# Kernel tuning notes

Hardware: AMD Instinct MI355X
Metric: run time of the kernel (lower is better)

The kernel has to match this reference:

```python
import jax, jax.numpy as jnp
import numpy as np

# dims
N, M, L, E = 50000, 1024, 3, 200000      # tgt nodes, src nodes, subtokens/node, edges
HID, EMB, VOCAB = 512, 256, 512
N_SLT, N_SRT = 4, 5                       # SLT edge types (messages), SRT edge types (output head)
W_SCALE = 0.02


def setup_inputs() -> dict:
    key = jax.random.key(0)
    ks = jax.random.split(key, 20)
    inp = {
        "tgt_x": jax.random.randint(ks[0], (N, L), 0, VOCAB),
        "x": jax.random.normal(ks[1], (M, HID), jnp.float32),
        "tgt_edge_index": jax.random.randint(ks[2], (2, E), 0, N),
        "tgt_edge_type": jax.random.randint(ks[3], (E,), 0, N_SLT),
        "embed_table": jax.random.normal(ks[4], (VOCAB, EMB), jnp.float32) * W_SCALE,
        # GCN layer 1 (called twice in the original forward) and layer 3 params
        "W_h1": jax.random.normal(ks[5], (EMB, EMB), jnp.float32) * W_SCALE,
        "W_rel1": jax.random.normal(ks[6], (N_SLT, EMB, EMB), jnp.float32) * W_SCALE,
        "W_src1": jax.random.normal(ks[7], (HID, EMB), jnp.float32) * W_SCALE,
        "W_h3": jax.random.normal(ks[8], (EMB, EMB), jnp.float32) * W_SCALE,
        "W_rel3": jax.random.normal(ks[9], (N_SLT, EMB, EMB), jnp.float32) * W_SCALE,
        "W_src3": jax.random.normal(ks[10], (HID, EMB), jnp.float32) * W_SCALE,
        # output heads
        "Wz": jax.random.normal(ks[11], (EMB, VOCAB), jnp.float32) * W_SCALE,
        "bz": jnp.zeros((VOCAB,), jnp.float32),
        "Wg": jax.random.normal(ks[12], (2 * EMB, N_SRT), jnp.float32) * W_SCALE,
        "bg": jnp.zeros((N_SRT,), jnp.float32),
    }
    return inp


def _gcn_layer(x_src, h, edge_index, edge_type, W_h, W_rel, W_src):
    """Relational GCN decoder layer with cross-attention to encoder nodes."""
    k = x_src @ W_src                                   # [M, EMB]
    attn = jax.nn.softmax(h @ k.T / jnp.sqrt(jnp.float32(EMB)), axis=1)  # [N, M]
    ctx = attn @ k                                      # [N, EMB]
    # per-edge-type transform first ([N, T, EMB]), then gather per edge
    h_t = jnp.einsum('nd,tdf->ntf', h, W_rel)           # [N, N_SLT, EMB]
    src, tgt = edge_index[0], edge_index[1]
    msg = h_t[src, edge_type]                           # [E, EMB] gather
    agg = jax.ops.segment_sum(msg, tgt, num_segments=h.shape[0])  # [N, EMB]
    return jax.nn.relu(h @ W_h + agg + ctx)


def reference(tgt_x, x, tgt_edge_index, tgt_edge_type, embed_table,
              W_h1, W_rel1, W_src1, W_h3, W_rel3, W_src3, Wz, bz, Wg, bg):
    # embedding + reduction over subtokens
    h = embed_table[tgt_x].sum(axis=1)                  # [N, EMB]
    # original code calls gcn1 twice, then gcn3 (gcn2 unused in training path)
    h = _gcn_layer(x, h, tgt_edge_index, tgt_edge_type, W_h1, W_rel1, W_src1)
    h = _gcn_layer(x, h, tgt_edge_index, tgt_edge_type, W_h1, W_rel1, W_src1)
    h = _gcn_layer(x, h, tgt_edge_index, tgt_edge_type, W_h3, W_rel3, W_src3)
    # node head
    node_pred = jax.nn.log_softmax(h @ Wz + bz, axis=1)  # [N, VOCAB]
    # edge head: gather [2,E,EMB] -> permute -> [E, 2*EMB]
    ef = h[tgt_edge_index]                               # [2, E, EMB]
    ef = jnp.transpose(ef, (1, 0, 2)).reshape(E, 2 * EMB)
    edge_pred = jax.nn.log_softmax(ef @ Wg + bg, axis=1)  # [E, N_SRT]
    return node_pred, edge_pred
```

## Files before the change

kernel.cpp:

```cpp
#include <hip/hip_runtime.h>
#include <hip/hip_bf16.h>
#include <cstdint>

#define N_NODES 50000
#define M_SRC   1024
#define E_EDGES 200000
#define EMB     256
#define HIDN    512
#define VOCABSZ 512
#define KW      1280

typedef __attribute__((ext_vector_type(8))) short bf16x8;
typedef __attribute__((ext_vector_type(4))) short bf16x4;
typedef __attribute__((ext_vector_type(4))) float f32x4;

__device__ inline short f2b(float f) {
    __hip_bfloat16 b = __float2bfloat16(f);
    return *reinterpret_cast<short*>(&b);
}
__device__ inline float b2f(short s) {
    __hip_bfloat16 b = *reinterpret_cast<__hip_bfloat16*>(&s);
    return __bfloat162float(b);
}

__device__ inline void gload16(const void* g, void* l) {
    __builtin_amdgcn_global_load_lds(
        (const __attribute__((address_space(1))) unsigned int*)g,
        (__attribute__((address_space(3))) unsigned int*)l,
        16, 0, 0);
}

__device__ inline void tr_read2(unsigned addr, bf16x4& lo, bf16x4& hi) {
    asm volatile("ds_read_b64_tr_b16 %0, %2\n\tds_read_b64_tr_b16 %1, %2 offset:512"
                 : "=&v"(lo), "=&v"(hi) : "v"(addr));
}

__global__ void embed_kernel(const int* __restrict__ tgt_x,
                             const float* __restrict__ table,
                             short* __restrict__ h)
{
    int n = blockIdx.x, d = threadIdx.x;
    const int* tx = tgt_x + (size_t)n * 3;
    float s = table[(size_t)tx[0] * EMB + d]
            + table[(size_t)tx[1] * EMB + d]
            + table[(size_t)tx[2] * EMB + d];
    h[(size_t)n * EMB + d] = f2b(s);
}

__global__ void convert_kernel(const float* __restrict__ in, short* __restrict__ out, int n)
{
    int i = blockIdx.x * 256 + threadIdx.x;
    if (i * 4 < n) {
        float4 v = *(const float4*)&in[i * 4];
        short4 o;
        o.x = f2b(v.x); o.y = f2b(v.y); o.z = f2b(v.z); o.w = f2b(v.w);
        *(short4*)&out[i * 4] = o;
    }
}

template<typename TIN>
__global__ void transpose_kernel(const TIN* __restrict__ in, short* __restrict__ out, int R, int C)
{
    __shared__ float t[32][33];
    int tx = threadIdx.x & 31, ty = threadIdx.x >> 5;
    int r0 = blockIdx.y * 32, c0 = blockIdx.x * 32;
#pragma unroll
    for (int i = 0; i < 4; i++) {
        int r = ty + i * 8;
        TIN v = in[(size_t)(r0 + r) * C + c0 + tx];
        if constexpr (sizeof(TIN) == 4) t[r][tx] = v;
        else                            t[r][tx] = b2f(v);
    }
    __syncthreads();
#pragma unroll
    for (int i = 0; i < 4; i++) {
        int r = ty + i * 8;
        out[(size_t)(c0 + r) * R + r0 + tx] = f2b(t[tx][r]);
    }
}

__global__ void transposeW_kernel(const float* __restrict__ Wh1, const float* __restrict__ Wh3,
                                  const float* __restrict__ Wr1, const float* __restrict__ Wr3,
                                  short* __restrict__ Wcat1, short* __restrict__ Wcat3)
{
    __shared__ float t[32][33];
    const int z = blockIdx.z;
    const float* in; short* outp; int coloff;
    if (z == 0)      { in = Wh1;                               outp = Wcat1; coloff = 0; }
    else if (z == 1) { in = Wh3;                               outp = Wcat3; coloff = 0; }
    else if (z < 6)  { in = Wr1 + (size_t)(z - 2) * EMB * EMB; outp = Wcat1; coloff = 256 + (z - 2) * 256; }
    else             { in = Wr3 + (size_t)(z - 6) * EMB * EMB; outp = Wcat3; coloff = 256 + (z - 6) * 256; }
    int tx = threadIdx.x & 31, ty = threadIdx.x >> 5;
    int r0 = blockIdx.y * 32, c0 = blockIdx.x * 32;
#pragma unroll
    for (int i = 0; i < 4; i++) {
        int r = ty + i * 8;
        t[r][tx] = in[(size_t)(r0 + r) * EMB + c0 + tx];
    }
    __syncthreads();
#pragma unroll
    for (int i = 0; i < 4; i++) {
        int r = ty + i * 8;
        outp[(size_t)(c0 + r) * KW + coloff + r0 + tx] = f2b(t[tx][r]);
    }
}

template<int MODE>
__global__ __launch_bounds__(256) void mgemm(
    const short* __restrict__ A, const short* __restrict__ BT,
    void* __restrict__ outp, const float* __restrict__ aux,
    const float* __restrict__ bias, int NR, int K, int J)
{
    __shared__ short As[128 * 40];
    __shared__ short Bs[128 * 40];
    const int tid  = threadIdx.x;
    const int n0   = blockIdx.x * 128;
    const int j0   = blockIdx.y * 128;
    const int lane = tid & 63, wid = tid >> 6;
    const int wr   = wid >> 1, wc = wid & 1;

    f32x4 acc[4][4];
#pragma unroll
    for (int m = 0; m < 4; m++)
#pragma unroll
        for (int n = 0; n < 4; n++) acc[m][n] = (f32x4){0.f, 0.f, 0.f, 0.f};

    for (int kt = 0; kt < K; kt += 32) {
#pragma unroll
        for (int r = 0; r < 2; r++) {
            int idx = tid + r * 256;
            int row = idx >> 2, ko = (idx & 3) * 8;
            int n = n0 + row;
            bf16x8 av = {0, 0, 0, 0, 0, 0, 0, 0};
            if (n < NR) av = *(const bf16x8*)&A[(size_t)n * K + kt + ko];
            *(bf16x8*)&As[row * 40 + ko] = av;
            *(bf16x8*)&Bs[row * 40 + ko] = *(const bf16x8*)&BT[(size_t)(j0 + row) * K + kt + ko];
        }
        __syncthreads();
        bf16x8 af[4], bfr[4];
#pragma unroll
        for (int m = 0; m < 4; m++)
            af[m] = *(const bf16x8*)&As[(wr * 64 + m * 16 + (lane & 15)) * 40 + (lane >> 4) * 8];
#pragma unroll
        for (int n = 0; n < 4; n++)
            bfr[n] = *(const bf16x8*)&Bs[(wc * 64 + n * 16 + (lane & 15)) * 40 + (lane >> 4) * 8];
#pragma unroll
        for (int m = 0; m < 4; m++)
#pragma unroll
            for (int n = 0; n < 4; n++)
                acc[m][n] = __builtin_amdgcn_mfma_f32_16x16x32_bf16(af[m], bfr[n], acc[m][n], 0, 0, 0);
        __syncthreads();
    }

#pragma unroll
    for (int m = 0; m < 4; m++) {
        int rbase = wr * 64 + m * 16 + ((lane >> 4) * 4);
#pragma unroll
        for (int r = 0; r < 4; r++) {
            int n_g = n0 + rbase + r;
            if (n_g >= NR) continue;
#pragma unroll
            for (int nn = 0; nn < 4; nn++) {
                int j_g = j0 + wc * 64 + nn * 16 + (lane & 15);
                ((short*)outp)[(size_t)n_g * J + j_g] = f2b(acc[m][nn][r]);
            }
        }
    }
}

__global__ __launch_bounds__(256) void mgemm_wide(
    const short* __restrict__ A1, const short* __restrict__ A2,
    const short* __restrict__ BT, short* __restrict__ outp,
    const float* __restrict__ aux, int NR)
{
    __shared__ short As[2][4096];
    __shared__ short Bs[2][16384];
    const int tid  = threadIdx.x;
    const int n0   = blockIdx.x * 64;
    const int lane = tid & 63, wid = tid >> 6;
    const int wr   = wid >> 1, wc = wid & 1;
    const int l4 = lane >> 4, l15 = lane & 15;

    auto SOFF = [](int r, int d8) {
        return (d8 & 1) * 8 + (r & 3) * 16 + ((r >> 3) & 3) * 64
             + ((r >> 2) & 1) * 256 + (d8 >> 1) * 512;
    };
    int a_row[2], a_d8[2];
#pragma unroll
    for (int q = 0; q < 2; q++) {
        int cig = tid + q * 256;
        int s = cig >> 8, ci = cig & 255;
        a_d8[q]  = (ci & 1) | (((ci >> 6) & 3) << 1);
        a_row[q] = s * 32 + (((ci >> 1) & 3) | (((ci >> 5) & 1) << 2) | (((ci >> 3) & 3) << 3));
    }
    int b_row[8], b_d8[8];
#pragma unroll
    for (int q = 0; q < 8; q++) {
        int cig = tid + q * 256;
        int s = cig >> 8, ci = cig & 255;
        b_d8[q]  = (ci & 1) | (((ci >> 6) & 3) << 1);
        b_row[q] = s * 32 + (((ci >> 1) & 3) | (((ci >> 5) & 1) << 2) | (((ci >> 3) & 3) << 3));
    }

    f32x4 acc[2][8];
#pragma unroll
    for (int m = 0; m < 2; m++)
#pragma unroll
        for (int n = 0; n < 8; n++) acc[m][n] = (f32x4){0.f, 0.f, 0.f, 0.f};

    auto STAGE = [&](int buf, int kt) {
#pragma unroll
        for (int q = 0; q < 2; q++) {
            int col = kt + a_d8[q] * 8;
            const short* src = (col < 256) ? &A1[(size_t)(n0 + a_row[q]) * 256 + col]
                                           : &A2[(size_t)(n0 + a_row[q]) * 1024 + (col - 256)];
            gload16(src, (char*)&As[buf][0] + q * 4096 + wid * 1024);
        }
#pragma unroll
        for (int q = 0; q < 8; q++) {
            gload16(&BT[(size_t)b_row[q] * KW + kt + b_d8[q] * 8],
                    (char*)&Bs[buf][0] + q * 4096 + wid * 1024);
        }
    };

    STAGE(0, 0);
    __syncthreads();

    for (int t = 0; t < 20; t++) {
        const int cur = t & 1;
        if (t + 1 < 20) STAGE(cur ^ 1, (t + 1) * 64);
#pragma unroll
        for (int kst = 0; kst < 2; kst++) {
            const int d8 = kst * 4 + l4;
            bf16x8 af[2], bfr[8];
#pragma unroll
            for (int m = 0; m < 2; m++)
                af[m] = *(const bf16x8*)&As[cur][wr * 2048 + SOFF(m * 16 + l15, d8)];
#pragma unroll
            for (int n = 0; n < 8; n++) {
                int sb = wc * 4 + (n >> 1);
                int r  = (n & 1) * 16 + l15;
                bfr[n] = *(const bf16x8*)&Bs[cur][sb * 2048 + SOFF(r, d8)];
            }
            __builtin_amdgcn_s_setprio(1);
#pragma unroll
            for (int m = 0; m < 2; m++)
#pragma unroll
                for (int n = 0; n < 8; n++)
                    acc[m][n] = __builtin_amdgcn_mfma_f32_16x16x32_bf16(af[m], bfr[n], acc[m][n], 0, 0, 0);
            __builtin_amdgcn_s_setprio(0);
        }
        __syncthreads();
    }

#pragma unroll
    for (int m = 0; m < 2; m++) {
        int rbase = wr * 32 + m * 16 + l4 * 4;
#pragma unroll
        for (int r = 0; r < 4; r++) {
            int n_g = n0 + rbase + r;
            if (n_g >= NR) continue;
#pragma unroll
            for (int nn = 0; nn < 8; nn++) {
                int j_g = wc * 128 + nn * 16 + l15;
                float v = acc[m][nn][r] + aux[(size_t)n_g * 256 + j_g];
                outp[(size_t)n_g * 256 + j_g] = f2b(fmaxf(v, 0.f));
            }
        }
    }
}

__global__ __launch_bounds__(128, 2) void attn_flash(
    const short* __restrict__ h, const short* __restrict__ kb,
    float* __restrict__ C, int NR)
{
    __shared__ short ks[2][32 * 256];
    __shared__ short Ps[64 * 36];

    const int tid = threadIdx.x;
    const int lane = tid & 63, wv = tid >> 6;
    const int l4 = lane >> 4, l15 = lane & 15;
    const int n0 = blockIdx.x * 64;

    auto LOFF = [](int key, int d8) {
        return (d8 & 1) * 8 + (key & 3) * 16 + ((key >> 3) & 3) * 64
             + ((key >> 2) & 1) * 256 + (d8 >> 1) * 512;
    };
    int keyq[8], d8q[8];
#pragma unroll
    for (int q = 0; q < 8; q++) {
        int ci = wv * 64 + lane + q * 128;
        d8q[q]  = (ci & 1) | ((ci >> 6) << 1);
        keyq[q] = ((ci >> 1) & 3) | (((ci >> 5) & 1) << 2) | (((ci >> 3) & 3) << 3);
    }

    bf16x8 hreg[2][8];
#pragma unroll
    for (int rg = 0; rg < 2; rg++) {
        int n = n0 + wv * 32 + rg * 16 + l15;
        const short* hp = &h[(size_t)(n < NR ? n : 0) * 256 + l4 * 8];
#pragma unroll
        for (int kst = 0; kst < 8; kst++) hreg[rg][kst] = *(const bf16x8*)&hp[kst * 32];
        if (n >= NR) {
#pragma unroll
            for (int kst = 0; kst < 8; kst++) hreg[rg][kst] = (bf16x8){0, 0, 0, 0, 0, 0, 0, 0};
        }
    }

#pragma unroll
    for (int q = 0; q < 8; q++)
        gload16(&kb[(size_t)keyq[q] * 256 + d8q[q] * 8],
                (char*)&ks[0][0] + q * 2048 + wv * 1024);
    __syncthreads();

    const unsigned ksbase = (unsigned)(uintptr_t)&ks[0][0];
    const unsigned trlane = 2u * (unsigned)(l15 + l4 * 64);

    f32x4 oacc[2][16];
#pragma unroll
    for (int rg = 0; rg < 2; rg++)
#pragma unroll
        for (int mm = 0; mm < 16; mm++) oacc[rg][mm] = (f32x4){0.f, 0.f, 0.f, 0.f};
    float lsum[2] = {0.f, 0.f};

    for (int c = 0; c < 32; c++) {
        const int cur = c & 1;
        if (c + 1 < 32) {
            const short* kbn = kb + (size_t)(c + 1) * 32 * 256;
#pragma unroll
            for (int q = 0; q < 8; q++)
                gload16(&kbn[(size_t)keyq[q] * 256 + d8q[q] * 8],
                        (char*)&ks[cur ^ 1][0] + q * 2048 + wv * 1024);
        }

        f32x4 sacc[2][2];
#pragma unroll
        for (int rg = 0; rg < 2; rg++) {
            sacc[rg][0] = (f32x4){0.f, 0.f, 0.f, 0.f};
            sacc[rg][1] = (f32x4){0.f, 0.f, 0.f, 0.f};
        }
        __builtin_amdgcn_s_setprio(1);
#pragma unroll
        for (int kst = 0; kst < 8; kst++) {
#pragma unroll
            for (int m = 0; m < 2; m++) {
                int krow = m * 16 + l15;
                bf16x8 afk = *(const bf16x8*)&ks[cur][LOFF(krow, kst * 4 + l4)];
                sacc[0][m] = __builtin_amdgcn_mfma_f32_16x16x32_bf16(afk, hreg[0][kst], sacc[0][m], 0, 0, 0);
                sacc[1][m] = __builtin_amdgcn_mfma_f32_16x16x32_bf16(afk, hreg[1][kst], sacc[1][m], 0, 0, 0);
            }
        }
        __builtin_amdgcn_s_setprio(0);

#pragma unroll
        for (int rg = 0; rg < 2; rg++) {
            int prow = wv * 32 + rg * 16 + l15;
            float psum = 0.f;
#pragma unroll
            for (int m = 0; m < 2; m++) {
                float p0 = __expf(sacc[rg][m][0] * 0.0625f);
                float p1 = __expf(sacc[rg][m][1] * 0.0625f);
                float p2 = __expf(sacc[rg][m][2] * 0.0625f);
                float p3 = __expf(sacc[rg][m][3] * 0.0625f);
                psum += (p0 + p1) + (p2 + p3);
                short4 pk;
                pk.x = f2b(p0); pk.y = f2b(p1); pk.z = f2b(p2); pk.w = f2b(p3);
                *(short4*)&Ps[prow * 36 + m * 16 + l4 * 4] = pk;
            }
            psum += __shfl_xor(psum, 16);
            psum += __shfl_xor(psum, 32);
            lsum[rg] += psum;
        }

        bf16x8 bf2[2];
#pragma unroll
        for (int rg = 0; rg < 2; rg++)
            bf2[rg] = *(const bf16x8*)&Ps[(wv * 32 + rg * 16 + l15) * 36 + l4 * 8];
        unsigned trb = ksbase + (unsigned)(cur * 16384) + trlane;
#pragma unroll
        for (int g = 0; g < 2; g++) {
            bf16x4 lo[8], hi[8];
#pragma unroll
            for (int q = 0; q < 8; q++)
                tr_read2(trb + (unsigned)((g * 8 + q) * 1024), lo[q], hi[q]);
            asm volatile("s_waitcnt lgkmcnt(0)" ::: "memory");
            __builtin_amdgcn_sched_barrier(0);
            __builtin_amdgcn_s_setprio(1);
#pragma unroll
            for (int q = 0; q < 8; q++) {
                bf16x8 af2;
#pragma unroll
                for (int t2 = 0; t2 < 4; t2++) { af2[t2] = lo[q][t2]; af2[t2 + 4] = hi[q][t2]; }
                oacc[0][g * 8 + q] = __builtin_amdgcn_mfma_f32_16x16x32_bf16(af2, bf2[0], oacc[0][g * 8 + q], 0, 0, 0);
                oacc[1][g * 8 + q] = __builtin_amdgcn_mfma_f32_16x16x32_bf16(af2, bf2[1], oacc[1][g * 8 + q], 0, 0, 0);
            }
            __builtin_amdgcn_s_setprio(0);
        }

        __syncthreads();
    }

#pragma unroll
    for (int rg = 0; rg < 2; rg++) {
        float li = 1.0f / lsum[rg];
        int hr = n0 + wv * 32 + rg * 16 + l15;
        if (hr >= NR) continue;
#pragma unroll
        for (int mm = 0; mm < 16; mm++) {
            float4 v;
            v.x = oacc[rg][mm][0] * li;
            v.y = oacc[rg][mm][1] * li;
            v.z = oacc[rg][mm][2] * li;
            v.w = oacc[rg][mm][3] * li;
            *(float4*)&C[(size_t)hr * 256 + mm * 16 + l4 * 4] = v;
        }
    }
}

__global__ void hist_kernel(const int* __restrict__ ei, int* __restrict__ deg)
{
    int e = blockIdx.x * 256 + threadIdx.x;
    if (e < E_EDGES) atomicAdd(&deg[ei[E_EDGES + e]], 1);
}

__global__ void scan1_kernel(const int* __restrict__ deg, int* __restrict__ incl,
                             int* __restrict__ bsum)
{
    __shared__ int s[256];
    int i = blockIdx.x * 256 + threadIdx.x;
    int v = (i < N_NODES) ? deg[i] : 0;
    s[threadIdx.x] = v;
    __syncthreads();
#pragma unroll
    for (int off = 1; off < 256; off <<= 1) {
        int t = (threadIdx.x >= off) ? s[threadIdx.x - off] : 0;
        __syncthreads();
        s[threadIdx.x] += t;
        __syncthreads();
    }
    if (i < N_NODES) incl[i] = s[threadIdx.x];
    if (threadIdx.x == 255) bsum[blockIdx.x] = s[255];
}

__global__ void scan2_kernel(int* __restrict__ bsum, int nb)
{
    __shared__ int s[256];
    int v = (threadIdx.x < nb) ? bsum[threadIdx.x] : 0;
    s[threadIdx.x] = v;
    __syncthreads();
#pragma unroll
    for (int off = 1; off < 256; off <<= 1) {
        int t = (threadIdx.x >= off) ? s[threadIdx.x - off] : 0;
        __syncthreads();
        s[threadIdx.x] += t;
        __syncthreads();
    }
    if (threadIdx.x < nb) bsum[threadIdx.x] = s[threadIdx.x];
}

__global__ void scan3_kernel(const int* __restrict__ deg, const int* __restrict__ incl,
                             const int* __restrict__ bsum, int* __restrict__ row_ptr,
                             int* __restrict__ cursor)
{
    int i = blockIdx.x * 256 + threadIdx.x;
    if (i >= N_NODES) return;
    int pref = (blockIdx.x > 0) ? bsum[blockIdx.x - 1] : 0;
    int start = pref + incl[i] - deg[i];
    row_ptr[i] = start;
    cursor[i]  = start;
    if (i == N_NODES - 1) row_ptr[N_NODES] = pref + incl[i];
}

__global__ void fill_kernel(const int* __restrict__ ei, const int* __restrict__ et,
                            int* __restrict__ cursor, int* __restrict__ eidx)
{
    int e = blockIdx.x * 256 + threadIdx.x;
    if (e >= E_EDGES) return;
    int tg = ei[E_EDGES + e];
    int slot = atomicAdd(&cursor[tg], 1);
    eidx[slot] = ei[e] | (et[e] << 16);
}

__global__ void agg2_kernel(const int* __restrict__ row_ptr, const int* __restrict__ eidx,
                            const short* __restrict__ h, short* __restrict__ Bagg)
{
    int w = (blockIdx.x * 256 + threadIdx.x) >> 6;
    if (w >= N_NODES) return;
    int lane = threadIdx.x & 63;
    int s0 = row_ptr[w], s1 = row_ptr[w + 1];
    float a0[4] = {0, 0, 0, 0}, a1[4] = {0, 0, 0, 0}, a2[4] = {0, 0, 0, 0}, a3[4] = {0, 0, 0, 0};
    for (int i = s0; i < s1; i++) {
        int p = eidx[i];
        int s = p & 0xFFFF, t = p >> 16;
        short4 g = *(const short4*)&h[(size_t)s * EMB + lane * 4];
        float f0 = b2f(g.x), f1 = b2f(g.y), f2 = b2f(g.z), f3 = b2f(g.w);
        if (t == 0)      { a0[0] += f0; a0[1] += f1; a0[2] += f2; a0[3] += f3; }
        else if (t == 1) { a1[0] += f0; a1[1] += f1; a1[2] += f2; a1[3] += f3; }
        else if (t == 2) { a2[0] += f0; a2[1] += f1; a2[2] += f2; a2[3] += f3; }
        else             { a3[0] += f0; a3[1] += f1; a3[2] += f2; a3[3] += f3; }
    }
    short4 o;
    o.x = f2b(a0[0]); o.y = f2b(a0[1]); o.z = f2b(a0[2]); o.w = f2b(a0[3]);
    *(short4*)&Bagg[(size_t)w * 1024 + 0 * 256 + lane * 4] = o;
    o.x = f2b(a1[0]); o.y = f2b(a1[1]); o.z = f2b(a1[2]); o.w = f2b(a1[3]);
    *(short4*)&Bagg[(size_t)w * 1024 + 1 * 256 + lane * 4] = o;
    o.x = f2b(a2[0]); o.y = f2b(a2[1]); o.z = f2b(a2[2]); o.w = f2b(a2[3]);
    *(short4*)&Bagg[(size_t)w * 1024 + 2 * 256 + lane * 4] = o;
    o.x = f2b(a3[0]); o.y = f2b(a3[1]); o.z = f2b(a3[2]); o.w = f2b(a3[3]);
    *(short4*)&Bagg[(size_t)w * 1024 + 3 * 256 + lane * 4] = o;
}

__global__ __launch_bounds__(512, 2) void head_kernel(
    const short* __restrict__ hmat, const short* __restrict__ WzT,
    const float* __restrict__ bz, float* __restrict__ out, int NR)
{
    __shared__ short hs[64 * 256];
    __shared__ float redm[64 * 8];
    __shared__ float reds[64 * 8];

    const int tid = threadIdx.x;
    const int lane = tid & 63, wv = tid >> 6;
    const int l4 = lane >> 4, l15 = lane & 15;
    const int n0 = blockIdx.x * 64;

#pragma unroll
    for (int i = 0; i < 4; i++) {
        int idx = tid + i * 512;
        int row = idx >> 5, kg = idx & 31;
        bf16x8 v = {0, 0, 0, 0, 0, 0, 0, 0};
        if (n0 + row < NR) v = *(const bf16x8*)&hmat[(size_t)(n0 + row) * 256 + kg * 8];
        *(bf16x8*)&hs[(row * 256 + kg * 8) ^ ((row & 7) << 3)] = v;
    }
    __syncthreads();

    f32x4 acc[4][4];
#pragma unroll
    for (int m = 0; m < 4; m++)
#pragma unroll
        for (int n = 0; n < 4; n++) acc[m][n] = (f32x4){0.f, 0.f, 0.f, 0.f};

#pragma unroll
    for (int kt = 0; kt < 256; kt += 32) {
        bf16x8 af[4], bfr[4];
#pragma unroll
        for (int m = 0; m < 4; m++) {
            int row = m * 16 + l15;
            af[m] = *(const bf16x8*)&hs[(row * 256 + kt + l4 * 8) ^ ((row & 7) << 3)];
        }
#pragma unroll
        for (int n = 0; n < 4; n++) {
            int col = wv * 64 + n * 16 + l15;
            bfr[n] = *(const bf16x8*)&WzT[(size_t)col * 256 + kt + l4 * 8];
        }
#pragma unroll
        for (int m = 0; m < 4; m++)
#pragma unroll
            for (int n = 0; n < 4; n++)
                acc[m][n] = __builtin_amdgcn_mfma_f32_16x16x32_bf16(af[m], bfr[n], acc[m][n], 0, 0, 0);
    }

    float bcol[4];
#pragma unroll
    for (int n = 0; n < 4; n++) bcol[n] = bz[wv * 64 + n * 16 + l15];
#pragma unroll
    for (int m = 0; m < 4; m++)
#pragma unroll
        for (int n = 0; n < 4; n++)
#pragma unroll
            for (int r = 0; r < 4; r++) acc[m][n][r] += bcol[n];

    float lg[4][4];
#pragma unroll
    for (int m = 0; m < 4; m++)
#pragma unroll
        for (int r = 0; r < 4; r++) {
            float v = fmaxf(fmaxf(acc[m][0][r], acc[m][1][r]), fmaxf(acc[m][2][r], acc[m][3][r]));
            v = fmaxf(v, __shfl_xor(v, 1));
            v = fmaxf(v, __shfl_xor(v, 2));
            v = fmaxf(v, __shfl_xor(v, 4));
            v = fmaxf(v, __shfl_xor(v, 8));
            if (l15 == 0) redm[(m * 16 + l4 * 4 + r) * 8 + wv] = v;
        }
    __syncthreads();
#pragma unroll
    for (int m = 0; m < 4; m++)
#pragma unroll
        for (int r = 0; r < 4; r++) {
            int row = m * 16 + l4 * 4 + r;
            float v = redm[row * 8 + 0];
#pragma unroll
            for (int w = 1; w < 8; w++) v = fmaxf(v, redm[row * 8 + w]);
            lg[m][r] = v;
        }
#pragma unroll
    for (int m = 0; m < 4; m++)
#pragma unroll
        for (int r = 0; r < 4; r++) {
            float gm = lg[m][r];
            float s = __expf(acc[m][0][r] - gm) + __expf(acc[m][1][r] - gm)
                    + __expf(acc[m][2][r] - gm) + __expf(acc[m][3][r] - gm);
            s += __shfl_xor(s, 1);
            s += __shfl_xor(s, 2);
            s += __shfl_xor(s, 4);
            s += __shfl_xor(s, 8);
            if (l15 == 0) reds[(m * 16 + l4 * 4 + r) * 8 + wv] = s;
        }
    __syncthreads();
#pragma unroll
    for (int m = 0; m < 4; m++)
#pragma unroll
        for (int r = 0; r < 4; r++) {
            int row = m * 16 + l4 * 4 + r;
            float s = reds[row * 8 + 0];
#pragma unroll
            for (int w = 1; w < 8; w++) s += reds[row * 8 + w];
            lg[m][r] += __logf(s);
        }
#pragma unroll
    for (int m = 0; m < 4; m++)
#pragma unroll
        for (int r = 0; r < 4; r++) {
            int hr = n0 + m * 16 + l4 * 4 + r;
            if (hr >= NR) continue;
#pragma unroll
            for (int n = 0; n < 4; n++)
                out[(size_t)hr * VOCABSZ + wv * 64 + n * 16 + l15] = acc[m][n][r] - lg[m][r];
        }
}

__global__ __launch_bounds__(256) void nodeproj_kernel(
    const short* __restrict__ h, const float* __restrict__ Wg,
    float* __restrict__ eproj)
{
    int lane = threadIdx.x & 63;
    int gw   = (blockIdx.x * 256 + threadIdx.x) >> 6;
    int nw   = (gridDim.x * 256) >> 6;
    float ws[4][5], wt[4][5];
#pragma unroll
    for (int c = 0; c < 4; c++)
#pragma unroll
        for (int j = 0; j < 5; j++) {
            ws[c][j] = Wg[(size_t)(lane * 4 + c) * 5 + j];
            wt[c][j] = Wg[(size_t)(256 + lane * 4 + c) * 5 + j];
        }

    for (int n = gw; n < N_NODES; n += nw) {
        short4 hv = *(const short4*)&h[(size_t)n * EMB + lane * 4];
        float f[4] = { b2f(hv.x), b2f(hv.y), b2f(hv.z), b2f(hv.w) };
        float a[5] = {0, 0, 0, 0, 0}, b[5] = {0, 0, 0, 0, 0};
#pragma unroll
        for (int c = 0; c < 4; c++)
#pragma unroll
            for (int j = 0; j < 5; j++) {
                a[j] += f[c] * ws[c][j];
                b[j] += f[c] * wt[c][j];
            }
#pragma unroll
        for (int j = 0; j < 5; j++)
#pragma unroll
            for (int off = 32; off; off >>= 1) {
                a[j] += __shfl_xor(a[j], off);
                b[j] += __shfl_xor(b[j], off);
            }
        if (lane == 0) {
#pragma unroll
            for (int j = 0; j < 5; j++) {
                eproj[(size_t)n * 10 + j]     = a[j];
                eproj[(size_t)n * 10 + 5 + j] = b[j];
            }
        }
    }
}

__global__ void edge_lsm_kernel(const int* __restrict__ ei,
                                const float* __restrict__ eproj,
                                const float* __restrict__ bg,
                                float* __restrict__ out)
{
    int e = blockIdx.x * 256 + threadIdx.x;
    if (e >= E_EDGES) return;
    int s = ei[e], t = ei[E_EDGES + e];
    const float* ps = &eproj[(size_t)s * 10];
    const float* pt = &eproj[(size_t)t * 10 + 5];
    float z[5];
#pragma unroll
    for (int j = 0; j < 5; j++) z[j] = ps[j] + pt[j] + bg[j];
    float mm = fmaxf(fmaxf(fmaxf(z[0], z[1]), fmaxf(z[2], z[3])), z[4]);
    float ss = __expf(z[0] - mm) + __expf(z[1] - mm) + __expf(z[2] - mm)
             + __expf(z[3] - mm) + __expf(z[4] - mm);
    float lg = mm + __logf(ss);
    float* o = &out[(size_t)e * 5];
#pragma unroll
    for (int j = 0; j < 5; j++) o[j] = z[j] - lg;
}

extern "C" void kernel_launch(void* const* d_in, const int* in_sizes, int n_in,
                              void* d_out, int out_size, void* d_ws, size_t ws_size,
                              hipStream_t stream)
{
    const int*   tgt_x = (const int*)  d_in[0];
    const float* x     = (const float*)d_in[1];
    const int*   ei    = (const int*)  d_in[2];
    const int*   et    = (const int*)  d_in[3];
    const float* table = (const float*)d_in[4];
    const float* Wh1   = (const float*)d_in[5];
    const float* Wrel1 = (const float*)d_in[6];
    const float* Wsrc1 = (const float*)d_in[7];
    const float* Wh3   = (const float*)d_in[8];
    const float* Wrel3 = (const float*)d_in[9];
    const float* Wsrc3 = (const float*)d_in[10];
    const float* Wz    = (const float*)d_in[11];
    const float* bz    = (const float*)d_in[12];
    const float* Wg    = (const float*)d_in[13];
    const float* bg    = (const float*)d_in[14];
    float* out = (float*)d_out;

    short* h_a = (short*)d_ws;
    short* h_b = h_a + (size_t)N_NODES * EMB;
    float* C   = (float*)(h_b + (size_t)N_NODES * EMB);
    short* Bagg = (short*)(C + (size_t)N_NODES * EMB);
    short* k1b = Bagg + (size_t)N_NODES * 1024;
    short* k3b = k1b + M_SRC * EMB;
    short* x_b = k3b + M_SRC * EMB;
    short* WsT1 = x_b + M_SRC * HIDN;
    short* WsT3 = WsT1 + EMB * HIDN;
    short* Wcat1 = WsT3 + EMB * HIDN;
    short* Wcat3 = Wcat1 + EMB * KW;
    short* WzT  = Wcat3 + EMB * KW;
    int* deg     = (int*)(WzT + VOCABSZ * EMB);
    int* incl    = deg + N_NODES;
    int* bsum    = incl + N_NODES;
    int* row_ptr = bsum + 256;
    int* cursor  = row_ptr + N_NODES + 1;
    int* eidx    = cursor + N_NODES;
    float* eproj = (float*)(eidx + E_EDGES);

    const int gN = (N_NODES + 127) / 128;
    const int gN64 = (N_NODES + 63) / 64;
    const int nb1 = (N_NODES + 255) / 256;

    hipMemsetAsync(deg, 0, N_NODES * sizeof(int), stream);
    hist_kernel<<<(E_EDGES + 255) / 256, 256, 0, stream>>>(ei, deg);
    scan1_kernel<<<nb1, 256, 0, stream>>>(deg, incl, bsum);
    scan2_kernel<<<1, 256, 0, stream>>>(bsum, nb1);
    scan3_kernel<<<nb1, 256, 0, stream>>>(deg, incl, bsum, row_ptr, cursor);
    fill_kernel<<<(E_EDGES + 255) / 256, 256, 0, stream>>>(ei, et, cursor, eidx);

    convert_kernel<<<(M_SRC * HIDN / 4 + 255) / 256, 256, 0, stream>>>(x, x_b, M_SRC * HIDN);
    transpose_kernel<float><<<dim3(EMB / 32, HIDN / 32), 256, 0, stream>>>(Wsrc1, WsT1, HIDN, EMB);
    transpose_kernel<float><<<dim3(EMB / 32, HIDN / 32), 256, 0, stream>>>(Wsrc3, WsT3, HIDN, EMB);
    transposeW_kernel<<<dim3(8, 8, 10), 256, 0, stream>>>(Wh1, Wh3, Wrel1, Wrel3, Wcat1, Wcat3);
    transpose_kernel<float><<<dim3(VOCABSZ / 32, EMB / 32), 256, 0, stream>>>(Wz, WzT, EMB, VOCABSZ);

    mgemm<0><<<dim3(M_SRC / 128, EMB / 128), 256, 0, stream>>>(x_b, WsT1, k1b, nullptr, nullptr, M_SRC, HIDN, EMB);
    mgemm<0><<<dim3(M_SRC / 128, EMB / 128), 256, 0, stream>>>(x_b, WsT3, k3b, nullptr, nullptr, M_SRC, HIDN, EMB);

    embed_kernel<<<N_NODES, 256, 0, stream>>>(tgt_x, table, h_a);

    short* h_cur = h_a;
    short* h_nxt = h_b;
    for (int layer = 0; layer < 3; layer++) {
        const short* kb   = (layer < 2) ? k1b   : k3b;
        const short* Wcat = (layer < 2) ? Wcat1 : Wcat3;

        attn_flash<<<gN64, 128, 0, stream>>>(h_cur, kb, C, N_NODES);
        agg2_kernel<<<(N_NODES + 3) / 4, 256, 0, stream>>>(row_ptr, eidx, h_cur, Bagg);
        mgemm_wide<<<dim3(gN64, 1), 256, 0, stream>>>(h_cur, Bagg, Wcat, h_nxt, C, N_NODES);
        short* tmp = h_cur; h_cur = h_nxt; h_nxt = tmp;
    }

    head_kernel<<<gN64, 512, 0, stream>>>(h_cur, WzT, bz, out, N_NODES);

    nodeproj_kernel<<<2048, 256, 0, stream>>>(h_cur, Wg, eproj);
    edge_lsm_kernel<<<(E_EDGES + 255) / 256, 256, 0, stream>>>(ei, eproj, bg,
                                                               out + (size_t)N_NODES * VOCABSZ);
}
```

Before: 769.7 us.

## Fuse edge aggregation into the wide GEMM A-tile staging via per-type CSR

Builds the CSR keyed by (target node, edge type) buckets instead of by target node. The separate aggregation kernel and its large bf16 Bagg intermediate are removed. mgemm_wide now gathers and sums neighbour rows of h directly while staging the aggregated part of the A operand into LDS. This avoids writing and re-reading a 50000x1024 buffer every layer, but it puts dependent, irregular global loads (row_ptr, eidx, h) and synchronous LDS stores into the GEMM's double-buffered pipeline, which may stall the MFMA loop.

```diff
diff --git a/kernel.cpp b/kernel.cpp
--- a/kernel.cpp
+++ b/kernel.cpp
@@ -9,6 +9,7 @@
 #define HIDN    512
 #define VOCABSZ 512
 #define KW      1280
+#define NB2     (N_NODES * 4)
 
 typedef __attribute__((ext_vector_type(8))) short bf16x8;
 typedef __attribute__((ext_vector_type(4))) short bf16x4;
@@ -169,9 +170,9 @@
 }
 
 __global__ __launch_bounds__(256) void mgemm_wide(
-    const short* __restrict__ A1, const short* __restrict__ A2,
-    const short* __restrict__ BT, short* __restrict__ outp,
-    const float* __restrict__ aux, int NR)
+    const short* __restrict__ A1, const short* __restrict__ BT,
+    short* __restrict__ outp, const float* __restrict__ aux,
+    const int* __restrict__ row_ptr2, const int* __restrict__ eidx2, int NR)
 {
     __shared__ short As[2][4096];
     __shared__ short Bs[2][16384];
@@ -209,12 +210,34 @@
         for (int n = 0; n < 8; n++) acc[m][n] = (f32x4){0.f, 0.f, 0.f, 0.f};
 
     auto STAGE = [&](int buf, int kt) {
-#pragma unroll
-        for (int q = 0; q < 2; q++) {
-            int col = kt + a_d8[q] * 8;
-            const short* src = (col < 256) ? &A1[(size_t)(n0 + a_row[q]) * 256 + col]
-                                           : &A2[(size_t)(n0 + a_row[q]) * 1024 + (col - 256)];
-            gload16(src, (char*)&As[buf][0] + q * 4096 + wid * 1024);
+        if (kt < 256) {
+#pragma unroll
+            for (int q = 0; q < 2; q++) {
+                gload16(&A1[(size_t)(n0 + a_row[q]) * 256 + kt + a_d8[q] * 8],
+                        (char*)&As[buf][0] + q * 4096 + wid * 1024);
+            }
+        } else {
+#pragma unroll
+            for (int q = 0; q < 2; q++) {
+                int n = n0 + a_row[q];
+                int col = kt + a_d8[q] * 8 - 256;
+                int ty = col >> 8, d = col & 255;
+                float a8[8] = {0.f, 0.f, 0.f, 0.f, 0.f, 0.f, 0.f, 0.f};
+                if (n < NR) {
+                    int bkt = n * 4 + ty;
+                    int i0 = row_ptr2[bkt], i1 = row_ptr2[bkt + 1];
+                    for (int i = i0; i < i1; i++) {
+                        int src = eidx2[i];
+                        bf16x8 v = *(const bf16x8*)&A1[(size_t)src * 256 + d];
+#pragma unroll
+                        for (int j = 0; j < 8; j++) a8[j] += b2f(v[j]);
+                    }
+                }
+                bf16x8 o;
+#pragma unroll
+                for (int j = 0; j < 8; j++) o[j] = f2b(a8[j]);
+                *(bf16x8*)((char*)&As[buf][0] + q * 4096 + wid * 1024 + lane * 16) = o;
+            }
         }
 #pragma unroll
         for (int q = 0; q < 8; q++) {
@@ -417,97 +440,69 @@
     }
 }
 
-__global__ void hist_kernel(const int* __restrict__ ei, int* __restrict__ deg)
+__global__ void hist2_kernel(const int* __restrict__ ei, const int* __restrict__ et,
+                             int* __restrict__ deg2)
 {
     int e = blockIdx.x * 256 + threadIdx.x;
-    if (e < E_EDGES) atomicAdd(&deg[ei[E_EDGES + e]], 1);
-}
-
-__global__ void scan1_kernel(const int* __restrict__ deg, int* __restrict__ incl,
-                             int* __restrict__ bsum)
-{
-    __shared__ int s[256];
-    int i = blockIdx.x * 256 + threadIdx.x;
-    int v = (i < N_NODES) ? deg[i] : 0;
+    if (e < E_EDGES) atomicAdd(&deg2[ei[E_EDGES + e] * 4 + et[e]], 1);
+}
+
+__global__ void scan1x_kernel(const int* __restrict__ deg2, int* __restrict__ incl2,
+                              int* __restrict__ bsum)
+{
+    __shared__ int s[1024];
+    int i = blockIdx.x * 1024 + threadIdx.x;
+    int v = (i < NB2) ? deg2[i] : 0;
     s[threadIdx.x] = v;
     __syncthreads();
 #pragma unroll
-    for (int off = 1; off < 256; off <<= 1) {
-        int t = (threadIdx.x >= off) ? s[threadIdx.x - off] : 0;
+    for (int off = 1; off < 1024; off <<= 1) {
+        int t = (threadIdx.x >= (unsigned)off) ? s[threadIdx.x - off] : 0;
         __syncthreads();
         s[threadIdx.x] += t;
         __syncthreads();
     }
-    if (i < N_NODES) incl[i] = s[threadIdx.x];
-    if (threadIdx.x == 255) bsum[blockIdx.x] = s[255];
+    if (i < NB2) incl2[i] = s[threadIdx.x];
+    if (threadIdx.x == 1023) bsum[blockIdx.x] = s[1023];
 }
 
 __global__ void scan2_kernel(int* __restrict__ bsum, int nb)
 {
     __shared__ int s[256];
-    int v = (threadIdx.x < nb) ? bsum[threadIdx.x] : 0;
+    int v = (threadIdx.x < (unsigned)nb) ? bsum[threadIdx.x] : 0;
     s[threadIdx.x] = v;
     __syncthreads();
 #pragma unroll
     for (int off = 1; off < 256; off <<= 1) {
-        int t = (threadIdx.x >= off) ? s[threadIdx.x - off] : 0;
+        int t = (threadIdx.x >= (unsigned)off) ? s[threadIdx.x - off] : 0;
         __syncthreads();
         s[threadIdx.x] += t;
         __syncthreads();
     }
-    if (threadIdx.x < nb) bsum[threadIdx.x] = s[threadIdx.x];
-}
-
-__global__ void scan3_kernel(const int* __restrict__ deg, const int* __restrict__ incl,
-                             const int* __restrict__ bsum, int* __restrict__ row_ptr,
-                             int* __restrict__ cursor)
-{
-    int i = blockIdx.x * 256 + threadIdx.x;
-    if (i >= N_NODES) return;
+    if (threadIdx.x < (unsigned)nb) bsum[threadIdx.x] = s[threadIdx.x];
+}
+
+__global__ void scan3x_kernel(const int* __restrict__ deg2, const int* __restrict__ incl2,
+                              const int* __restrict__ bsum, int* __restrict__ row_ptr2,
+                              int* __restrict__ cursor2)
+{
+    int i = blockIdx.x * 1024 + threadIdx.x;
+    if (i >= NB2) return;
     int pref = (blockIdx.x > 0) ? bsum[blockIdx.x - 1] : 0;
-    int start = pref + incl[i] - deg[i];
-    row_ptr[i] = start;
-    cursor[i]  = start;
-    if (i == N_NODES - 1) row_ptr[N_NODES] = pref + incl[i];
-}
-
-__global__ void fill_kernel(const int* __restrict__ ei, const int* __restrict__ et,
-                            int* __restrict__ cursor, int* __restrict__ eidx)
+    int start = pref + incl2[i] - deg2[i];
+    row_ptr2[i] = start;
+    cursor2[i]  = start;
+    if (i == NB2 - 1) row_ptr2[NB2] = pref + incl2[i];
+}
+
+__global__ void fill2_kernel(const int* __restrict__ ei, const int* __restrict__ et,
+                             int* __restrict__ cursor2, int* __restrict__ eidx2)
 {
     int e = blockIdx.x * 256 + threadIdx.x;
     if (e >= E_EDGES) return;
-    int tg = ei[E_EDGES + e];
-    int slot = atomicAdd(&cursor[tg], 1);
-    eidx[slot] = ei[e] | (et[e] << 16);
-}
-
-__global__ void agg2_kernel(const int* __restrict__ row_ptr, const int* __restrict__ eidx,
-                            const short* __restrict__ h, short* __restrict__ Bagg)
-{
-    int w = (blockIdx.x * 256 + threadIdx.x) >> 6;
-    if (w >= N_NODES) return;
-    int lane = threadIdx.x & 63;
-    int s0 = row_ptr[w], s1 = row_ptr[w + 1];
-    float a0[4] = {0, 0, 0, 0}, a1[4] = {0, 0, 0, 0}, a2[4] = {0, 0, 0, 0}, a3[4] = {0, 0, 0, 0};
-    for (int i = s0; i < s1; i++) {
-        int p = eidx[i];
-        int s = p & 0xFFFF, t = p >> 16;
-        short4 g = *(const short4*)&h[(size_t)s * EMB + lane * 4];
-        float f0 = b2f(g.x), f1 = b2f(g.y), f2 = b2f(g.z), f3 = b2f(g.w);
-        if (t == 0)      { a0[0] += f0; a0[1] += f1; a0[2] += f2; a0[3] += f3; }
-        else if (t == 1) { a1[0] += f0; a1[1] += f1; a1[2] += f2; a1[3] += f3; }
-        else if (t == 2) { a2[0] += f0; a2[1] += f1; a2[2] += f2; a2[3] += f3; }
-        else             { a3[0] += f0; a3[1] += f1; a3[2] += f2; a3[3] += f3; }
-    }
-    short4 o;
-    o.x = f2b(a0[0]); o.y = f2b(a0[1]); o.z = f2b(a0[2]); o.w = f2b(a0[3]);
-    *(short4*)&Bagg[(size_t)w * 1024 + 0 * 256 + lane * 4] = o;
-    o.x = f2b(a1[0]); o.y = f2b(a1[1]); o.z = f2b(a1[2]); o.w = f2b(a1[3]);
-    *(short4*)&Bagg[(size_t)w * 1024 + 1 * 256 + lane * 4] = o;
-    o.x = f2b(a2[0]); o.y = f2b(a2[1]); o.z = f2b(a2[2]); o.w = f2b(a2[3]);
-    *(short4*)&Bagg[(size_t)w * 1024 + 2 * 256 + lane * 4] = o;
-    o.x = f2b(a3[0]); o.y = f2b(a3[1]); o.z = f2b(a3[2]); o.w = f2b(a3[3]);
-    *(short4*)&Bagg[(size_t)w * 1024 + 3 * 256 + lane * 4] = o;
+    int b = ei[E_EDGES + e] * 4 + et[e];
+    int slot = atomicAdd(&cursor2[b], 1);
+    eidx2[slot] = ei[e];
 }
 
 __global__ __launch_bounds__(512, 2) void head_kernel(
@@ -718,8 +713,7 @@
     short* h_a = (short*)d_ws;
     short* h_b = h_a + (size_t)N_NODES * EMB;
     float* C   = (float*)(h_b + (size_t)N_NODES * EMB);
-    short* Bagg = (short*)(C + (size_t)N_NODES * EMB);
-    short* k1b = Bagg + (size_t)N_NODES * 1024;
+    short* k1b = (short*)(C + (size_t)N_NODES * EMB);
     short* k3b = k1b + M_SRC * EMB;
     short* x_b = k3b + M_SRC * EMB;
     short* WsT1 = x_b + M_SRC * HIDN;
@@ -727,24 +721,23 @@
     short* Wcat1 = WsT3 + EMB * HIDN;
     short* Wcat3 = Wcat1 + EMB * KW;
     short* WzT  = Wcat3 + EMB * KW;
-    int* deg     = (int*)(WzT + VOCABSZ * EMB);
-    int* incl    = deg + N_NODES;
-    int* bsum    = incl + N_NODES;
-    int* row_ptr = bsum + 256;
-    int* cursor  = row_ptr + N_NODES + 1;
-    int* eidx    = cursor + N_NODES;
-    float* eproj = (float*)(eidx + E_EDGES);
-
-    const int gN = (N_NODES + 127) / 128;
+    int* deg2     = (int*)(WzT + VOCABSZ * EMB);
+    int* incl2    = deg2 + NB2;
+    int* bsum     = incl2 + NB2;
+    int* row_ptr2 = bsum + 256;
+    int* cursor2  = row_ptr2 + NB2 + 1;
+    int* eidx2    = cursor2 + NB2;
+    float* eproj  = (float*)(eidx2 + E_EDGES);
+
     const int gN64 = (N_NODES + 63) / 64;
-    const int nb1 = (N_NODES + 255) / 256;
-
-    hipMemsetAsync(deg, 0, N_NODES * sizeof(int), stream);
-    hist_kernel<<<(E_EDGES + 255) / 256, 256, 0, stream>>>(ei, deg);
-    scan1_kernel<<<nb1, 256, 0, stream>>>(deg, incl, bsum);
-    scan2_kernel<<<1, 256, 0, stream>>>(bsum, nb1);
-    scan3_kernel<<<nb1, 256, 0, stream>>>(deg, incl, bsum, row_ptr, cursor);
-    fill_kernel<<<(E_EDGES + 255) / 256, 256, 0, stream>>>(ei, et, cursor, eidx);
+    const int nb2 = (NB2 + 1023) / 1024;
+
+    hipMemsetAsync(deg2, 0, NB2 * sizeof(int), stream);
+    hist2_kernel<<<(E_EDGES + 255) / 256, 256, 0, stream>>>(ei, et, deg2);
+    scan1x_kernel<<<nb2, 1024, 0, stream>>>(deg2, incl2, bsum);
+    scan2_kernel<<<1, 256, 0, stream>>>(bsum, nb2);
+    scan3x_kernel<<<nb2, 1024, 0, stream>>>(deg2, incl2, bsum, row_ptr2, cursor2);
+    fill2_kernel<<<(E_EDGES + 255) / 256, 256, 0, stream>>>(ei, et, cursor2, eidx2);
 
     convert_kernel<<<(M_SRC * HIDN / 4 + 255) / 256, 256, 0, stream>>>(x, x_b, M_SRC * HIDN);
     transpose_kernel<float><<<dim3(EMB / 32, HIDN / 32), 256, 0, stream>>>(Wsrc1, WsT1, HIDN, EMB);
@@ -764,8 +757,8 @@
         const short* Wcat = (layer < 2) ? Wcat1 : Wcat3;
 
         attn_flash<<<gN64, 128, 0, stream>>>(h_cur, kb, C, N_NODES);
-        agg2_kernel<<<(N_NODES + 3) / 4, 256, 0, stream>>>(row_ptr, eidx, h_cur, Bagg);
-        mgemm_wide<<<dim3(gN64, 1), 256, 0, stream>>>(h_cur, Bagg, Wcat, h_nxt, C, N_NODES);
+        mgemm_wide<<<dim3(gN64, 1), 256, 0, stream>>>(h_cur, Wcat, h_nxt, C,
+                                                      row_ptr2, eidx2, N_NODES);
         short* tmp = h_cur; h_cur = h_nxt; h_nxt = tmp;
     }
 
```

New measurement: 1.011 ms. +31.3%, slower.
